# Optimization experiments

Hardware: AMD Instinct MI355X
Metric: run time of the kernel (lower is better)

## Reference

```python
import jax, jax.numpy as jnp
import numpy as np

N = 50000          # total nodes across the batched graphs
E = 800000         # edges (before self-loops)
D_IN = 128         # input_dim
D_H = 128          # hidden_channels
N_CLASSES = 2
N_GRAPHS = 64


def setup_inputs() -> dict:
    key = jax.random.key(0)
    ks = jax.random.split(key, 9)
    x = jax.random.normal(ks[0], (N, D_IN), dtype=jnp.float32)
    edge_index = jax.random.randint(ks[1], (2, E), 0, N, dtype=jnp.int64)
    batch = jnp.sort(jax.random.randint(ks[2], (N,), 0, N_GRAPHS, dtype=jnp.int64))
    s1 = 1.0 / np.sqrt(D_IN)
    s2 = 1.0 / np.sqrt(D_H)
    W1 = jax.random.uniform(ks[3], (D_IN, D_H), jnp.float32, -s1, s1)
    b1 = jnp.zeros((D_H,), jnp.float32)
    W2 = jax.random.uniform(ks[4], (D_H, D_H), jnp.float32, -s2, s2)
    b2 = jnp.zeros((D_H,), jnp.float32)
    Wfc = jax.random.uniform(ks[5], (D_H, N_CLASSES), jnp.float32, -s2, s2)
    bfc = jnp.zeros((N_CLASSES,), jnp.float32)
    return {"x": x, "edge_index": edge_index, "batch": batch,
            "W1": W1, "b1": b1, "W2": W2, "b2": b2, "Wfc": Wfc, "bfc": bfc}


def _gcn_conv(x, src, dst, norm, W, b):
    # GCNConv: h = W x, then out_i = sum_{j->i} norm_ij * h_j + b
    h = x @ W                                   # [N, D]
    msg = h[src] * norm[:, None]                # gather + scale, [E+N, D]
    out = jax.ops.segment_sum(msg, dst, num_segments=N)
    return out + b


def reference(x, edge_index, batch, W1, b1, W2, b2, Wfc, bfc):
    loops = jnp.arange(N, dtype=edge_index.dtype)
    src = jnp.concatenate([edge_index[0], loops])  # add self-loops
    dst = jnp.concatenate([edge_index[1], loops])
    # symmetric normalization D^-1/2 (A+I) D^-1/2
    deg = jax.ops.segment_sum(jnp.ones_like(dst, x.dtype), dst, num_segments=N)
    dinv = jax.lax.rsqrt(deg)                      # deg >= 1 due to self-loops
    norm = dinv[src] * dinv[dst]                   # [E+N]

    h = jax.nn.relu(_gcn_conv(x, src, dst, norm, W1, b1))
    h = _gcn_conv(h, src, dst, norm, W2, b2)

    # global_mean_pool over graph ids
    summed = jax.ops.segment_sum(h, batch, num_segments=N_GRAPHS)
    counts = jax.ops.segment_sum(jnp.ones((N,), x.dtype), batch, num_segments=N_GRAPHS)
    pooled = summed / jnp.maximum(counts, 1.0)[:, None]

    return pooled @ Wfc + bfc                      # [N_GRAPHS, N_CLASSES]
```

## Files before the change

### kernel.cpp

```cpp
#include <hip/hip_runtime.h>
#include <hip/hip_fp16.h>


#define N_NODES 50000
#define N_EDGES 800000
#define ETOT (N_EDGES + N_NODES)
#define D 128
#define NG 64
#define NC 2
#define JT 128
#define NBLK_W ((N_NODES + JT - 1) / JT)
#define NODES_PAD (NBLK_W * JT)
#define WT_F4 (NODES_PAD * NG / 4)
#define Q_F4 (NG * D / 4)

__global__ void k_init(int* __restrict__ deg, float4* __restrict__ wT4,
                       float4* __restrict__ q4, float* __restrict__ cnt,
                       int* __restrict__ cursor) {
    int i = blockIdx.x * 256 + threadIdx.x;
    float4 z = {0.f, 0.f, 0.f, 0.f};
    if (i < WT_F4) wT4[i] = z;
    if (i < Q_F4)  q4[i] = z;
    if (i < N_NODES) deg[i] = 1;
    if (i < NG)    cnt[i] = 0.f;
    if (i == 0)    *cursor = 0;
}

__global__ void k_deg(const int* __restrict__ ei, int* __restrict__ deg) {
    int e = blockIdx.x * 256 + threadIdx.x;
    if (e < N_EDGES) atomicAdd(&deg[ei[N_EDGES + e]], 1);
}

__global__ __launch_bounds__(256) void k_off(const int* __restrict__ deg,
                                             int* __restrict__ cursor,
                                             int* __restrict__ off,
                                             int* __restrict__ cur,
                                             float* __restrict__ dinv,
                                             const int* __restrict__ batch,
                                             float* __restrict__ cnt) {
    __shared__ int sh[256];
    __shared__ int base;
    __shared__ float scnt[NG];
    int t = threadIdx.x;
    int n = blockIdx.x * 256 + t;
    if (t < NG) scnt[t] = 0.f;
    int dg = (n < N_NODES) ? deg[n] : 0;
    sh[t] = dg;
    __syncthreads();
    for (int o = 1; o < 256; o <<= 1) {
        int u = (t >= o) ? sh[t - o] : 0;
        __syncthreads();
        sh[t] += u;
        __syncthreads();
    }
    if (t == 255) base = atomicAdd(cursor, sh[255]);
    __syncthreads();
    if (n < N_NODES) {
        int o2 = base + sh[t] - dg;
        off[n] = o2;
        cur[n] = o2;
        dinv[n] = rsqrtf((float)dg);
        atomicAdd(&scnt[batch[n]], 1.f);
    }
    __syncthreads();
    if (t < NG) {
        float v = scnt[t];
        if (v > 0.f) atomicAdd(&cnt[t], v);
    }
}

__global__ void k_scatter(const int* __restrict__ ei, int* __restrict__ cur,
                          int* __restrict__ csr) {
    int e = blockIdx.x * 256 + threadIdx.x;
    if (e >= ETOT) return;
    int s, d2;
    if (e < N_EDGES) { s = ei[e]; d2 = ei[N_EDGES + e]; }
    else             { s = e - N_EDGES; d2 = s; }
    csr[atomicAdd(&cur[d2], 1)] = s;
}

__global__ void k_wacc(const int* __restrict__ ei,
                       const float* __restrict__ dinv,
                       const int* __restrict__ batch,
                       float* __restrict__ wT) {
    int e = blockIdx.x * 256 + threadIdx.x;
    if (e >= ETOT) return;
    int s, d2;
    if (e < N_EDGES) { s = ei[e]; d2 = ei[N_EDGES + e]; }
    else             { s = e - N_EDGES; d2 = s; }
    atomicAdd(&wT[(size_t)s * NG + batch[d2]], dinv[s] * dinv[d2]);
}

__global__ __launch_bounds__(256) void k_gemm(const float* __restrict__ A,
                                              const float* __restrict__ W,
                                              __half* __restrict__ C) {
    __shared__ float As[128][68];
    int tid = threadIdx.x;
    int row0 = blockIdx.x * 64;
    {
        int r  = tid >> 2;
        int f4 = tid & 3;
        int ra = row0 + r; if (ra >= N_NODES) ra = N_NODES - 1;
        const float* arow = A + (size_t)ra * D;
#pragma unroll 1
        for (int i = 0; i < 8; i++) {
            int k0 = f4 * 4 + i * 16;
            float4 v = *(const float4*)(arow + k0);
            As[k0 + 0][r] = v.x;
            As[k0 + 1][r] = v.y;
            As[k0 + 2][r] = v.z;
            As[k0 + 3][r] = v.w;
        }
    }
    __syncthreads();

    int tx = tid & 15;
    int ty = tid >> 4;
    float acc[4][8];
#pragma unroll
    for (int i = 0; i < 4; i++)
#pragma unroll
        for (int j = 0; j < 8; j++) acc[i][j] = 0.f;

    const float* wp = W + tx * 8;
#pragma unroll 4
    for (int k = 0; k < 128; k++) {
        float4 a  = *(const float4*)&As[k][ty * 4];
        float4 b0 = *(const float4*)(wp + k * 128);
        float4 b1 = *(const float4*)(wp + k * 128 + 4);
        float av[4] = {a.x, a.y, a.z, a.w};
        float bv[8] = {b0.x, b0.y, b0.z, b0.w, b1.x, b1.y, b1.z, b1.w};
#pragma unroll
        for (int i = 0; i < 4; i++)
#pragma unroll
            for (int j = 0; j < 8; j++) acc[i][j] = fmaf(av[i], bv[j], acc[i][j]);
    }

#pragma unroll 1
    for (int i = 0; i < 4; i++) {
        int r = row0 + ty * 4 + i;
        if (r < N_NODES) {
            __half2 hh[4];
#pragma unroll
            for (int k2 = 0; k2 < 4; k2++)
                hh[k2] = __floats2half2_rn(acc[i][2 * k2], acc[i][2 * k2 + 1]);
            *(float4*)(C + (size_t)r * D + tx * 8) = *(float4*)hh;
        }
    }
}

__global__ __launch_bounds__(256) void k_agg(const __half* __restrict__ h,
                                             const int* __restrict__ off,
                                             const int* __restrict__ deg,
                                             const int* __restrict__ csr,
                                             const float* __restrict__ dinv,
                                             const float* __restrict__ bias,
                                             float* __restrict__ outp) {
    int n    = (blockIdx.x * 256 + threadIdx.x) >> 6;
    int lane = threadIdx.x & 63;
    if (n >= N_NODES) return;
    int beg = off[n], end = beg + deg[n];
    float dn = dinv[n];
    const __half2* hb = (const __half2*)h + lane;

    float ax = 0.f, ay = 0.f, bx = 0.f, by = 0.f;
    float cx = 0.f, cy = 0.f, dx = 0.f, dy = 0.f;
    int p = beg;
    for (; p + 8 <= end; p += 8) {
        int s0 = csr[p],     s1 = csr[p + 1], s2 = csr[p + 2], s3 = csr[p + 3];
        int s4 = csr[p + 4], s5 = csr[p + 5], s6 = csr[p + 6], s7 = csr[p + 7];
        float w0 = dinv[s0], w1 = dinv[s1], w2 = dinv[s2], w3 = dinv[s3];
        float w4 = dinv[s4], w5 = dinv[s5], w6 = dinv[s6], w7 = dinv[s7];
        float2 v0 = __half22float2(hb[(size_t)s0 * 64]);
        float2 v1 = __half22float2(hb[(size_t)s1 * 64]);
        float2 v2 = __half22float2(hb[(size_t)s2 * 64]);
        float2 v3 = __half22float2(hb[(size_t)s3 * 64]);
        float2 v4 = __half22float2(hb[(size_t)s4 * 64]);
        float2 v5 = __half22float2(hb[(size_t)s5 * 64]);
        float2 v6 = __half22float2(hb[(size_t)s6 * 64]);
        float2 v7 = __half22float2(hb[(size_t)s7 * 64]);
        ax = fmaf(w0, v0.x, ax); ay = fmaf(w0, v0.y, ay);
        bx = fmaf(w1, v1.x, bx); by = fmaf(w1, v1.y, by);
        cx = fmaf(w2, v2.x, cx); cy = fmaf(w2, v2.y, cy);
        dx = fmaf(w3, v3.x, dx); dy = fmaf(w3, v3.y, dy);
        ax = fmaf(w4, v4.x, ax); ay = fmaf(w4, v4.y, ay);
        bx = fmaf(w5, v5.x, bx); by = fmaf(w5, v5.y, by);
        cx = fmaf(w6, v6.x, cx); cy = fmaf(w6, v6.y, cy);
        dx = fmaf(w7, v7.x, dx); dy = fmaf(w7, v7.y, dy);
    }
    for (; p < end; p++) {
        int s = csr[p];
        float w = dinv[s];
        float2 v = __half22float2(hb[(size_t)s * 64]);
        ax = fmaf(w, v.x, ax); ay = fmaf(w, v.y, ay);
    }
    float ox = ((ax + bx) + (cx + dx)) * dn;
    float oy = ((ay + by) + (cy + dy)) * dn;

    ox = fmaxf(ox + bias[2 * lane], 0.f);
    oy = fmaxf(oy + bias[2 * lane + 1], 0.f);
    float2 o = {ox, oy};
    *(float2*)(outp + (size_t)n * D + 2 * lane) = o;
}

__global__ __launch_bounds__(256) void k_wgemm(const float* __restrict__ wT,
                                               const float* __restrict__ g,
                                               float* __restrict__ q) {
    __shared__ float ws[JT][NG];
    int t = threadIdx.x;
    int j0 = blockIdx.x * JT;
    {
        const float4* src = (const float4*)(wT + (size_t)j0 * NG);
        float4* dst = (float4*)ws;
        for (int i = t; i < JT * NG / 4; i += 256) dst[i] = src[i];
    }
    __syncthreads();
    int d  = t & 127;
    int bg = t >> 7;
    float acc[32];
#pragma unroll
    for (int i = 0; i < 32; i++) acc[i] = 0.f;
    int jlim = N_NODES - j0; if (jlim > JT) jlim = JT;
    for (int jj = 0; jj < jlim; jj++) {
        float gv = g[(size_t)(j0 + jj) * D + d];
        const float* wrow = &ws[jj][bg * 32];
#pragma unroll
        for (int i = 0; i < 32; i++)
            acc[i] = fmaf(wrow[i], gv, acc[i]);
    }
    float* qb = q + (size_t)(bg * 32) * D + d;
#pragma unroll
    for (int i = 0; i < 32; i++)
        atomicAdd(qb + (size_t)i * D, acc[i]);
}

__global__ void k_head(const float* __restrict__ q, const float* __restrict__ cnt,
                       const float* __restrict__ W2, const float* __restrict__ b2,
                       const float* __restrict__ Wfc, const float* __restrict__ bfc,
                       float* __restrict__ outp) {
    __shared__ float pooled[D];
    int b = blockIdx.x, t = threadIdx.x;
    float cn = cnt[b];
    float pv = 0.f;
    if (cn > 0.f) {
        float acc = 0.f;
        for (int k = 0; k < D; k++)
            acc = fmaf(q[b * D + k], W2[k * D + t], acc);
        pv = acc / cn + b2[t];
    }
    pooled[t] = pv;
    __syncthreads();
    if (t < NC) {
        float acc = bfc[t];
        for (int k = 0; k < D; k++)
            acc = fmaf(pooled[k], Wfc[k * NC + t], acc);
        outp[b * NC + t] = acc;
    }
}

extern "C" void kernel_launch(void* const* d_in, const int* in_sizes, int n_in,
                              void* d_out, int out_size, void* d_ws, size_t ws_size,
                              hipStream_t stream) {
    const float* x     = (const float*)d_in[0];
    const int*   ei    = (const int*)  d_in[1];
    const int*   batch = (const int*)  d_in[2];
    const float* W1    = (const float*)d_in[3];
    const float* b1    = (const float*)d_in[4];
    const float* W2    = (const float*)d_in[5];
    const float* b2    = (const float*)d_in[6];
    const float* Wfc   = (const float*)d_in[7];
    const float* bfc   = (const float*)d_in[8];
    float* out = (float*)d_out;

    char* w = (char*)d_ws;
    auto alloc = [&](size_t bytes) {
        char* p = w;
        w += (bytes + 255) & ~(size_t)255;
        return p;
    };
    int*    deg    = (int*)   alloc((size_t)N_NODES * 4);
    float*  dinv   = (float*) alloc((size_t)N_NODES * 4);
    int*    off    = (int*)   alloc((size_t)N_NODES * 4);
    int*    cur    = (int*)   alloc((size_t)N_NODES * 4);
    int*    csr    = (int*)   alloc((size_t)ETOT * 4);
    int*    cursor = (int*)   alloc(256);
    __half* hbuf   = (__half*)alloc((size_t)N_NODES * D * 2);
    float*  gbuf   = (float*) alloc((size_t)N_NODES * D * 4);
    float*  wT     = (float*) alloc((size_t)NODES_PAD * NG * 4);
    float*  q      = (float*) alloc((size_t)NG * D * 4);
    float*  cnt    = (float*) alloc((size_t)NG * 4);

    k_init<<<(WT_F4 + 255) / 256, 256, 0, stream>>>(deg, (float4*)wT, (float4*)q, cnt, cursor);
    k_deg<<<(N_EDGES + 255) / 256, 256, 0, stream>>>(ei, deg);
    k_off<<<(N_NODES + 255) / 256, 256, 0, stream>>>(deg, cursor, off, cur, dinv, batch, cnt);
    k_scatter<<<(ETOT + 255) / 256, 256, 0, stream>>>(ei, cur, csr);
    k_wacc<<<(ETOT + 255) / 256, 256, 0, stream>>>(ei, dinv, batch, wT);

    k_gemm<<<(N_NODES + 63) / 64, 256, 0, stream>>>(x, W1, hbuf);
    k_agg<<<(N_NODES * 64 + 255) / 256, 256, 0, stream>>>(hbuf, off, deg, csr, dinv, b1, gbuf);

    k_wgemm<<<NBLK_W, 256, 0, stream>>>(wT, gbuf, q);
    k_head<<<NG, 128, 0, stream>>>(q, cnt, W2, b2, Wfc, bfc, out);
}
```

Before: 293.5 us.

## Replace wgemm atomics with fp16 per-block partials and separate reduction kernel

The pooled weighted-sum kernel now uses a smaller node tile and a float4 register tile (8 graphs x 4 features per thread) with vectorized loads of g. Instead of float atomics into q from every block, each block writes fp16 partial sums to a staging buffer, and a new reduction kernel sums them in segments before a few atomics. The aim is to remove heavy atomic contention and improve load efficiency. The cost is an extra kernel launch, extra memory traffic, and precision loss from rounding the partials to half.

```diff
diff --git a/kernel.cpp b/kernel.cpp
--- a/kernel.cpp
+++ b/kernel.cpp
@@ -8,11 +8,12 @@
 #define D 128
 #define NG 64
 #define NC 2
-#define JT 128
+#define JT 64
 #define NBLK_W ((N_NODES + JT - 1) / JT)
 #define NODES_PAD (NBLK_W * JT)
 #define WT_F4 (NODES_PAD * NG / 4)
 #define Q_F4 (NG * D / 4)
+#define BSEG ((NBLK_W + 7) / 8)
 
 __global__ void k_init(int* __restrict__ deg, float4* __restrict__ wT4,
                        float4* __restrict__ q4, float* __restrict__ cnt,
@@ -205,7 +206,7 @@
 
 __global__ __launch_bounds__(256) void k_wgemm(const float* __restrict__ wT,
                                                const float* __restrict__ g,
-                                               float* __restrict__ q) {
+                                               __half* __restrict__ qp) {
     __shared__ float ws[JT][NG];
     int t = threadIdx.x;
     int j0 = blockIdx.x * JT;
@@ -215,23 +216,43 @@
         for (int i = t; i < JT * NG / 4; i += 256) dst[i] = src[i];
     }
     __syncthreads();
-    int d  = t & 127;
-    int bg = t >> 7;
-    float acc[32];
-#pragma unroll
-    for (int i = 0; i < 32; i++) acc[i] = 0.f;
+    int d4 = t & 31;
+    int gg = t >> 5;
+    float4 acc[8];
+#pragma unroll
+    for (int i = 0; i < 8; i++) acc[i] = make_float4(0.f, 0.f, 0.f, 0.f);
     int jlim = N_NODES - j0; if (jlim > JT) jlim = JT;
+#pragma unroll 4
     for (int jj = 0; jj < jlim; jj++) {
-        float gv = g[(size_t)(j0 + jj) * D + d];
-        const float* wrow = &ws[jj][bg * 32];
-#pragma unroll
-        for (int i = 0; i < 32; i++)
-            acc[i] = fmaf(wrow[i], gv, acc[i]);
-    }
-    float* qb = q + (size_t)(bg * 32) * D + d;
-#pragma unroll
-    for (int i = 0; i < 32; i++)
-        atomicAdd(qb + (size_t)i * D, acc[i]);
+        float4 gv = *(const float4*)(g + (size_t)(j0 + jj) * D + d4 * 4);
+        const float* wrow = &ws[jj][gg * 8];
+#pragma unroll
+        for (int i = 0; i < 8; i++) {
+            float w = wrow[i];
+            acc[i].x = fmaf(w, gv.x, acc[i].x);
+            acc[i].y = fmaf(w, gv.y, acc[i].y);
+            acc[i].z = fmaf(w, gv.z, acc[i].z);
+            acc[i].w = fmaf(w, gv.w, acc[i].w);
+        }
+    }
+    __half* base = qp + (size_t)blockIdx.x * (NG * D);
+#pragma unroll
+    for (int i = 0; i < 8; i++) {
+        __half2 hh[2];
+        hh[0] = __floats2half2_rn(acc[i].x, acc[i].y);
+        hh[1] = __floats2half2_rn(acc[i].z, acc[i].w);
+        *(float2*)(base + (gg * 8 + i) * D + d4 * 4) = *(float2*)hh;
+    }
+}
+
+__global__ void k_qred(const __half* __restrict__ qp, float* __restrict__ q) {
+    int i = blockIdx.x * 256 + threadIdx.x;
+    int b0 = blockIdx.y * BSEG;
+    int b1 = b0 + BSEG; if (b1 > NBLK_W) b1 = NBLK_W;
+    float s = 0.f;
+    const __half* p = qp + i;
+    for (int b = b0; b < b1; b++) s += __half2float(p[(size_t)b * NG * D]);
+    atomicAdd(&q[i], s);
 }
 
 __global__ void k_head(const float* __restrict__ q, const float* __restrict__ cnt,
@@ -287,6 +308,7 @@
     __half* hbuf   = (__half*)alloc((size_t)N_NODES * D * 2);
     float*  gbuf   = (float*) alloc((size_t)N_NODES * D * 4);
     float*  wT     = (float*) alloc((size_t)NODES_PAD * NG * 4);
+    __half* qp     = (__half*)alloc((size_t)NBLK_W * NG * D * 2);
     float*  q      = (float*) alloc((size_t)NG * D * 4);
     float*  cnt    = (float*) alloc((size_t)NG * 4);
 
@@ -299,6 +321,8 @@
     k_gemm<<<(N_NODES + 63) / 64, 256, 0, stream>>>(x, W1, hbuf);
     k_agg<<<(N_NODES * 64 + 255) / 256, 256, 0, stream>>>(hbuf, off, deg, csr, dinv, b1, gbuf);
 
-    k_wgemm<<<NBLK_W, 256, 0, stream>>>(wT, gbuf, q);
+    k_wgemm<<<NBLK_W, 256, 0, stream>>>(wT, gbuf, qp);
+    dim3 gr(32, 8);
+    k_qred<<<gr, 256, 0, stream>>>(qp, q);
     k_head<<<NG, 128, 0, stream>>>(q, cnt, W2, b2, Wfc, bfc, out);
 }
```

Result: faster. 284.1 us (-3.2%).
